# Kernel tuning notes

Hardware: AMD Instinct MI355X
Metric: run time of the kernel (lower is better)

Reference implementation:

```python
import jax, jax.numpy as jnp
import numpy as np

N_ENT = 100000
N_REL = 12
D = 64
E = 1000000
LAYER_DIMS = [64, 32]


def _xavier(key, shape):
    fan_in, fan_out = shape[-1], shape[-2] if len(shape) >= 2 else shape[-1]
    std = np.sqrt(2.0 / (fan_in + fan_out)).astype(np.float32)
    return jax.random.normal(key, shape, jnp.float32) * std


def setup_inputs() -> dict:
    key = jax.random.key(0)
    ks = jax.random.split(key, 14)
    return {
        "entity_emb": _xavier(ks[0], (N_ENT, D)),
        "rel_emb": _xavier(ks[1], (N_REL, D)),
        "W_r": _xavier(ks[2], (N_REL, D, D)),
        "W1_0_w": _xavier(ks[3], (LAYER_DIMS[0], D)),
        "W1_0_b": jnp.zeros((LAYER_DIMS[0],), jnp.float32),
        "W2_0_w": _xavier(ks[4], (LAYER_DIMS[0], D)),
        "W2_0_b": jnp.zeros((LAYER_DIMS[0],), jnp.float32),
        "W1_1_w": _xavier(ks[5], (LAYER_DIMS[1], LAYER_DIMS[0])),
        "W1_1_b": jnp.zeros((LAYER_DIMS[1],), jnp.float32),
        "W2_1_w": _xavier(ks[6], (LAYER_DIMS[1], LAYER_DIMS[0])),
        "W2_1_b": jnp.zeros((LAYER_DIMS[1],), jnp.float32),
        "src": jax.random.randint(ks[7], (E,), 0, N_ENT, jnp.int32),
        "dst": jax.random.randint(ks[8], (E,), 0, N_ENT, jnp.int32),
        "etype": jax.random.randint(ks[9], (E,), 0, N_REL, jnp.int32),
    }


def reference(entity_emb, rel_emb, W_r, W1_0_w, W1_0_b, W2_0_w, W2_0_b,
              W1_1_w, W1_1_b, W2_1_w, W2_1_b, src, dst, etype):
    n = entity_emb.shape[0]

    # --- compute_attention: per-edge TransR scores, edge_softmax over dst ---
    # Instead of gathering W_r[etype] per edge ([E,D,D] is huge), project every
    # node by every relation matrix once: [N, R, Dr].
    proj = jnp.einsum('nd,kdr->nkr', entity_emb, W_r)
    tail = proj[src, etype]          # [E, Dr] (src projected by its edge's W_r)
    head = proj[dst, etype]          # [E, Dr]
    rel = rel_emb[etype]             # [E, Dr]
    logits = jnp.sum(tail * jnp.tanh(head + rel), axis=-1)  # [E]

    # edge softmax grouped by destination node (stable)
    m = jax.ops.segment_max(logits, dst, num_segments=n)
    ex = jnp.exp(logits - m[dst])
    den = jax.ops.segment_sum(ex, dst, num_segments=n)
    att = ex / den[dst]              # [E]

    # --- KGATLayer: gather-scale-scatter + bi-interaction (dropout = 0) ---
    def layer(x, W1w, W1b, W2w, W2b):
        h_n = jax.ops.segment_sum(x[src] * att[:, None], dst, num_segments=n)
        add = jax.nn.leaky_relu((x + h_n) @ W1w.T + W1b)
        mul = jax.nn.leaky_relu((x * h_n) @ W2w.T + W2b)
        return add + mul

    x0 = entity_emb
    x1 = layer(x0, W1_0_w, W1_0_b, W2_0_w, W2_0_b)
    x2 = layer(x1, W1_1_w, W1_1_b, W2_1_w, W2_1_b)
    # embedder concatenates the input and every layer output
    return jnp.concatenate([x0, x1, x2], axis=1)  # [N, 64+64+32]
```

## Files before the change

kernel.cpp:

```cpp
#include <hip/hip_runtime.h>
#include <hip/hip_bf16.h>
#include <math.h>


typedef __attribute__((ext_vector_type(8))) short short8;
typedef __attribute__((ext_vector_type(4))) float float4v;

__device__ __forceinline__ short f2bf(float f) {
  __hip_bfloat16 h = __float2bfloat16(f);
  return *(short*)&h;
}
__device__ __forceinline__ float bf2f(short s) {
  return __uint_as_float(((unsigned)(unsigned short)s) << 16);
}

#define LOG2E 1.4426950408889634f
#define BS1_TILE 2048

__global__ void k_prep(const float* __restrict__ emb, short* __restrict__ emb_h,
                       float* __restrict__ out,
                       const float* __restrict__ Wr, short* __restrict__ Bt,
                       const float* __restrict__ W10, const float* __restrict__ W20,
                       const float* __restrict__ W11, const float* __restrict__ W21,
                       short* __restrict__ w1h0, short* __restrict__ w1l0,
                       short* __restrict__ w2h0, short* __restrict__ w2l0,
                       short* __restrict__ w1h1, short* __restrict__ w1l1,
                       short* __restrict__ w2h1, short* __restrict__ w2l1,
                       const int* __restrict__ src, const int* __restrict__ dst,
                       const int* __restrict__ et, int* __restrict__ bcur,
                       uint2* __restrict__ stg, int nE, int bsh, int cap,
                       int nb1, int nb_cvt, int n4) {
  __shared__ int hist[256];
  __shared__ int base[256];
  int b = blockIdx.x, t = threadIdx.x;
  if (b < nb1) {
    hist[t] = 0;
    __syncthreads();
    int tile = b * BS1_TILE;
#pragma unroll
    for (int j = 0; j < BS1_TILE / 256; j++) {
      int e = tile + j * 256 + t;
      if (e < nE) atomicAdd(&hist[dst[e] >> bsh], 1);
    }
    __syncthreads();
    int cnt = hist[t];
    if (cnt > 0) base[t] = atomicAdd(&bcur[t], cnt);
    hist[t] = 0;
    __syncthreads();
#pragma unroll
    for (int j = 0; j < BS1_TILE / 256; j++) {
      int e = tile + j * 256 + t;
      if (e < nE) {
        int d = dst[e], bk = d >> bsh;
        int r = atomicAdd(&hist[bk], 1);
        stg[(size_t)bk * cap + base[bk] + r] =
            make_uint2((unsigned)src[e], (unsigned)d | ((unsigned)et[e] << 20));
      }
    }
    return;
  }
  int b2 = b - nb1;
  if (b2 < nb_cvt) {
    int i = b2 * 256 + t;
    if (i < n4) {
      float4 v = ((const float4*)emb)[i];
      union { short s[4]; uint2 u; } o;
      o.s[0] = f2bf(v.x); o.s[1] = f2bf(v.y); o.s[2] = f2bf(v.z); o.s[3] = f2bf(v.w);
      ((uint2*)emb_h)[i] = o.u;
      int node = i >> 4, ch = i & 15;
      *(float4*)(out + (size_t)node * 160 + ch * 4) = v;
    }
  } else if (b2 < nb_cvt + 12) {
    int k = b2 - nb_cvt;
    for (int i = t; i < 4096; i += 256) {
      int d = i >> 6, r = i & 63;
      Bt[k * 4096 + r * 64 + d] = f2bf(Wr[k * 4096 + i]);
    }
  } else {
    int i = (b2 - nb_cvt - 12) * 256 + t;
    const float* W; short* H; short* L; int j;
    if (i < 4096) { W = W10; H = w1h0; L = w1l0; j = i; }
    else if (i < 8192) { W = W20; H = w2h0; L = w2l0; j = i - 4096; }
    else if (i < 10240) { W = W11; H = w1h1; L = w1l1; j = i - 8192; }
    else if (i < 12288) { W = W21; H = w2h1; L = w2l1; j = i - 10240; }
    else return;
    float w = W[j];
    short hi = f2bf(w);
    H[j] = hi;
    L[j] = f2bf(w - bf2f(hi));
  }
}

__global__ __launch_bounds__(256) void k_projb2(const short* __restrict__ A,
                                                const short* __restrict__ Bt,
                                                short* __restrict__ proj,
                                                int n_ent,
                                                const uint2* __restrict__ stg,
                                                const int* __restrict__ bcur,
                                                int* __restrict__ row_ptr,
                                                uint2* __restrict__ csr2,
                                                int nbg, int bsh, int cap,
                                                int nbuck, int nE) {
  __shared__ char smem[4 * 64 * 72 * 2];
  int bid = blockIdx.x, t = threadIdx.x;
  if (bid >= nbg) {
    int b = bid - nbg;
    int* cnt = (int*)smem;
    int* sc = cnt + 1024;
    int* bs = sc + 1024;
    int v = (t < nbuck) ? bcur[t] : 0;
    bs[t] = v;
    __syncthreads();
    for (int o = 1; o < 256; o <<= 1) {
      int a = (t >= o) ? bs[t - o] : 0;
      __syncthreads();
      bs[t] += a;
      __syncthreads();
    }
    int gbase = bs[b] - bcur[b];
    int n = n_ent;
    int lo = b << bsh;
    if (lo > n) lo = n;
    int hi = (b + 1) << bsh;
    if (hi > n) hi = n;
    int w = hi - lo;
#pragma unroll
    for (int j = 0; j < 4; j++) cnt[t + j * 256] = 0;
    __syncthreads();
    int m = bcur[b];
    const uint2* S = stg + (size_t)b * cap;
    for (int p = t; p < m; p += 256)
      atomicAdd(&cnt[(int)(S[p].y & 0xFFFFFu) - lo], 1);
    __syncthreads();
#pragma unroll
    for (int j = 0; j < 4; j++) sc[t + j * 256] = cnt[t + j * 256];
    __syncthreads();
    for (int o = 1; o < 1024; o <<= 1) {
      int a[4];
#pragma unroll
      for (int j = 0; j < 4; j++) {
        int i = t + j * 256;
        a[j] = (i >= o) ? sc[i - o] : 0;
      }
      __syncthreads();
#pragma unroll
      for (int j = 0; j < 4; j++) sc[t + j * 256] += a[j];
      __syncthreads();
    }
#pragma unroll
    for (int j = 0; j < 4; j++) {
      int i = t + j * 256;
      if (i < w) {
        int c0 = gbase + sc[i] - cnt[i];
        row_ptr[lo + i] = c0;
        cnt[i] = c0;
      }
    }
    if (b == nbuck - 1 && t == 0) row_ptr[n] = nE;
    __syncthreads();
    for (int p = t; p < m; p += 256) {
      uint2 vv = S[p];
      int d = (int)(vv.y & 0xFFFFFu);
      int pos = atomicAdd(&cnt[d - lo], 1);
      csr2[pos] = vv;
    }
    return;
  }
  int wave = t >> 6, lane = t & 63;
  int quad = lane >> 4, l16 = lane & 15;
  int m0 = bid * 256 + wave * 64;
  unsigned short* W = (unsigned short*)smem + wave * 64 * 72;
  short8 a[4][2];
#pragma unroll
  for (int mt = 0; mt < 4; mt++)
#pragma unroll
    for (int kc = 0; kc < 2; kc++) {
      int row = m0 + mt * 16 + l16;
      int rr = row < n_ent ? row : 0;
      a[mt][kc] = *(const short8*)(A + (size_t)rr * 64 + kc * 32 + quad * 8);
    }
  for (int k = 0; k < 12; k++) {
    const short* B = Bt + k * 4096;
    short8 b[4][2];
#pragma unroll
    for (int nt = 0; nt < 4; nt++)
#pragma unroll
      for (int kc = 0; kc < 2; kc++)
        b[nt][kc] = *(const short8*)(B + (nt * 16 + l16) * 64 + kc * 32 + quad * 8);
    float4v acc[4][4];
#pragma unroll
    for (int mt = 0; mt < 4; mt++)
#pragma unroll
      for (int nt = 0; nt < 4; nt++)
        acc[mt][nt] = (float4v){0.f, 0.f, 0.f, 0.f};
#pragma unroll
    for (int kc = 0; kc < 2; kc++)
#pragma unroll
      for (int mt = 0; mt < 4; mt++)
#pragma unroll
        for (int nt = 0; nt < 4; nt++)
          acc[mt][nt] = __builtin_amdgcn_mfma_f32_16x16x32_bf16(
              a[mt][kc], b[nt][kc], acc[mt][nt], 0, 0, 0);
#pragma unroll
    for (int mt = 0; mt < 4; mt++)
#pragma unroll
      for (int nt = 0; nt < 4; nt++)
#pragma unroll
        for (int r = 0; r < 4; r++) {
          int row = mt * 16 + quad * 4 + r;
          int col = nt * 16 + l16;
          W[row * 72 + col] = (unsigned short)f2bf(acc[mt][nt][r]);
        }
    const size_t plane = (size_t)k * n_ent;
#pragma unroll
    for (int i = 0; i < 8; i++) {
      int row = (lane >> 3) + 8 * i;
      int cs = (lane & 7) * 8;
      short8 v = *(const short8*)(W + row * 72 + cs);
      int node = m0 + row;
      if (node < n_ent)
        *(short8*)(proj + (plane + node) * 64 + cs) = v;
    }
  }
}

__global__ __launch_bounds__(256) void k_logits(const short* __restrict__ ps,
                                                const float* __restrict__ rel_emb,
                                                uint2* csr2, int nE, int n_ent) {
  int t = threadIdx.x;
  int lane = t & 63;
  int sub = lane >> 3;
  int c8 = (lane & 7) * 8;
  int e0 = (blockIdx.x * 4 + (t >> 6)) * 32;
  if (e0 >= nE) return;
  int ku[4];
  short8 tl[4], hd[4];
#pragma unroll
  for (int u = 0; u < 4; u++) {
    int e = e0 + u * 8 + sub;
    int ee = e < nE ? e : nE - 1;
    uint2 c = csr2[ee];
    int s = (int)c.x;
    int d = (int)(c.y & 0xFFFFFu);
    int k = (int)(c.y >> 20);
    ku[u] = k;
    const size_t plane = (size_t)k * n_ent;
    tl[u] = *(const short8*)(ps + (plane + s) * 64 + c8);
    hd[u] = *(const short8*)(ps + (plane + d) * 64 + c8);
  }
  float v[4];
#pragma unroll
  for (int u = 0; u < 4; u++) {
    const float* rp = rel_emb + ku[u] * 64 + c8;
    float4 r0 = *(const float4*)rp;
    float4 r1 = *(const float4*)(rp + 4);
    float rr[8] = {r0.x, r0.y, r0.z, r0.w, r1.x, r1.y, r1.z, r1.w};
    float vv = 0.f;
#pragma unroll
    for (int q = 0; q < 8; q++) {
      float x = bf2f(hd[u][q]) + rr[q];
      float tt = __builtin_amdgcn_exp2f(x * (2.f * LOG2E));
      float r = __builtin_amdgcn_rcpf(tt + 1.f);
      float th = fmaf(-2.f, r, 1.f);
      vv = fmaf(bf2f(tl[u][q]), th, vv);
    }
    vv += __shfl_xor(vv, 1);
    vv += __shfl_xor(vv, 2);
    vv += __shfl_xor(vv, 4);
    v[u] = __builtin_amdgcn_exp2f(vv * LOG2E);
  }
  int uu = lane & 7;
  if (uu < 4) {
    float myv = v[0];
    if (uu == 1) myv = v[1];
    if (uu == 2) myv = v[2];
    if (uu == 3) myv = v[3];
    int e = e0 + uu * 8 + sub;
    if (e < nE) csr2[e].y = __float_as_uint(myv);
  }
}

__global__ __launch_bounds__(256) void k_agg(const short* __restrict__ xh,
                                             const int* __restrict__ row_ptr,
                                             const uint2* __restrict__ csr,
                                             float* __restrict__ hn, int n_ent) {
  int wave = threadIdx.x >> 6, lane = threadIdx.x & 63;
  int n = blockIdx.x * 4 + wave;
  if (n >= n_ent) return;
  int jb = row_ptr[n], je = row_ptr[n + 1];
  int deg = je - jb;
  if (deg == 0) {
    hn[(size_t)n * 64 + lane] = 0.f;
    return;
  }
  uint2 c = (lane < deg) ? csr[jb + lane] : make_uint2(0u, 0u);
  int sidx = (int)c.x;
  float exv = (lane < deg) ? __uint_as_float(c.y) : 0.f;
  float den = exv;
#pragma unroll
  for (int o = 32; o; o >>= 1) den += __shfl_xor(den, o);
  int m = deg < 64 ? deg : 64;
  float acc = 0.f;
  for (int j = 0; j < m; j += 8) {
    int s0 = __shfl(sidx, j), s1 = __shfl(sidx, j + 1);
    int s2 = __shfl(sidx, j + 2), s3 = __shfl(sidx, j + 3);
    int s4 = __shfl(sidx, j + 4), s5 = __shfl(sidx, j + 5);
    int s6 = __shfl(sidx, j + 6), s7 = __shfl(sidx, j + 7);
    float e0 = __shfl(exv, j), e1 = __shfl(exv, j + 1);
    float e2 = __shfl(exv, j + 2), e3 = __shfl(exv, j + 3);
    float e4 = __shfl(exv, j + 4), e5 = __shfl(exv, j + 5);
    float e6 = __shfl(exv, j + 6), e7 = __shfl(exv, j + 7);
    short g0 = xh[(size_t)s0 * 64 + lane];
    short g1 = xh[(size_t)s1 * 64 + lane];
    short g2 = xh[(size_t)s2 * 64 + lane];
    short g3 = xh[(size_t)s3 * 64 + lane];
    short g4 = xh[(size_t)s4 * 64 + lane];
    short g5 = xh[(size_t)s5 * 64 + lane];
    short g6 = xh[(size_t)s6 * 64 + lane];
    short g7 = xh[(size_t)s7 * 64 + lane];
    acc = fmaf(e0, bf2f(g0), acc); acc = fmaf(e1, bf2f(g1), acc);
    acc = fmaf(e2, bf2f(g2), acc); acc = fmaf(e3, bf2f(g3), acc);
    acc = fmaf(e4, bf2f(g4), acc); acc = fmaf(e5, bf2f(g5), acc);
    acc = fmaf(e6, bf2f(g6), acc); acc = fmaf(e7, bf2f(g7), acc);
  }
  if (deg > 64) {
    for (int jj = jb + 64; jj < je; jj++) {
      uint2 cc = csr[jj];
      float ee = __uint_as_float(cc.y);
      den += ee;
      acc = fmaf(ee, bf2f(xh[(size_t)cc.x * 64 + lane]), acc);
    }
  }
  hn[(size_t)n * 64 + lane] = acc / den;
}

template <int OD, bool FIRST>
__global__ __launch_bounds__(256) void k_upmfma(const float* __restrict__ x,
                                                const float* __restrict__ hn,
                                                const short* __restrict__ g1h,
                                                const short* __restrict__ g1l,
                                                const short* __restrict__ g2h,
                                                const short* __restrict__ g2l,
                                                const float* __restrict__ b1,
                                                const float* __restrict__ b2,
                                                float* __restrict__ out,
                                                float* __restrict__ x_next,
                                                short* __restrict__ xh_next,
                                                int n_ent) {
  constexpr int NT = OD / 16;
  constexpr int S = (OD == 64) ? 66 : 34;
  __shared__ short wbuf[4 * OD * 72];
  short* w1h = wbuf;
  short* w1l = wbuf + OD * 72;
  short* w2h = wbuf + 2 * OD * 72;
  short* w2l = wbuf + 3 * OD * 72;
  int t = threadIdx.x;
  for (int i = t; i < OD * 16; i += 256) {
    int o = i >> 4, dq = (i & 15) * 4;
    *(uint2*)(w1h + o * 72 + dq) = *(const uint2*)(g1h + o * 64 + dq);
    *(uint2*)(w1l + o * 72 + dq) = *(const uint2*)(g1l + o * 64 + dq);
    *(uint2*)(w2h + o * 72 + dq) = *(const uint2*)(g2h + o * 64 + dq);
    *(uint2*)(w2l + o * 72 + dq) = *(const uint2*)(g2l + o * 64 + dq);
  }
  int wave = t >> 6, lane = t & 63;
  int quad = lane >> 4, l16 = lane & 15;
  int m0 = blockIdx.x * 128 + wave * 32;
  float4v accA[2][NT], accM[2][NT];
#pragma unroll
  for (int mt = 0; mt < 2; mt++)
#pragma unroll
    for (int nt = 0; nt < NT; nt++) {
      accA[mt][nt] = (float4v){0.f, 0.f, 0.f, 0.f};
      accM[mt][nt] = (float4v){0.f, 0.f, 0.f, 0.f};
    }
  __syncthreads();
#pragma unroll
  for (int kc = 0; kc < 2; kc++) {
    short8 ah_add[2], al_add[2], ah_mul[2], al_mul[2];
#pragma unroll
    for (int mt = 0; mt < 2; mt++) {
      int row = m0 + mt * 16 + l16;
      int rr = row < n_ent ? row : 0;
      const float* xp = x + (size_t)rr * 64 + kc * 32 + quad * 8;
      const float* hp = hn + (size_t)rr * 64 + kc * 32 + quad * 8;
      float4 xa = *(const float4*)xp;
      float4 xb = *(const float4*)(xp + 4);
      float4 ha = *(const float4*)hp;
      float4 hb = *(const float4*)(hp + 4);
      float xs[8] = {xa.x, xa.y, xa.z, xa.w, xb.x, xb.y, xb.z, xb.w};
      float hs[8] = {ha.x, ha.y, ha.z, ha.w, hb.x, hb.y, hb.z, hb.w};
#pragma unroll
      for (int q = 0; q < 8; q++) {
        float s = xs[q] + hs[q];
        short shi = f2bf(s);
        ah_add[mt][q] = shi;
        al_add[mt][q] = f2bf(s - bf2f(shi));
        float p = xs[q] * hs[q];
        short phi = f2bf(p);
        ah_mul[mt][q] = phi;
        al_mul[mt][q] = f2bf(p - bf2f(phi));
      }
    }
#pragma unroll
    for (int nt = 0; nt < NT; nt++) {
      int boff = (nt * 16 + l16) * 72 + kc * 32 + quad * 8;
      short8 b1h = *(const short8*)(w1h + boff);
      short8 b1l = *(const short8*)(w1l + boff);
      short8 b2h = *(const short8*)(w2h + boff);
      short8 b2l = *(const short8*)(w2l + boff);
#pragma unroll
      for (int mt = 0; mt < 2; mt++) {
        accA[mt][nt] = __builtin_amdgcn_mfma_f32_16x16x32_bf16(
            ah_add[mt], b1h, accA[mt][nt], 0, 0, 0);
        accA[mt][nt] = __builtin_amdgcn_mfma_f32_16x16x32_bf16(
            al_add[mt], b1h, accA[mt][nt], 0, 0, 0);
        accA[mt][nt] = __builtin_amdgcn_mfma_f32_16x16x32_bf16(
            ah_add[mt], b1l, accA[mt][nt], 0, 0, 0);
        accM[mt][nt] = __builtin_amdgcn_mfma_f32_16x16x32_bf16(
            ah_mul[mt], b2h, accM[mt][nt], 0, 0, 0);
        accM[mt][nt] = __builtin_amdgcn_mfma_f32_16x16x32_bf16(
            al_mul[mt], b2h, accM[mt][nt], 0, 0, 0);
        accM[mt][nt] = __builtin_amdgcn_mfma_f32_16x16x32_bf16(
            ah_mul[mt], b2l, accM[mt][nt], 0, 0, 0);
      }
    }
  }
  __syncthreads();
  float* yt = (float*)wbuf + wave * 32 * S;
#pragma unroll
  for (int nt = 0; nt < NT; nt++) {
    int col = nt * 16 + l16;
    float bb1 = b1[col], bb2 = b2[col];
#pragma unroll
    for (int mt = 0; mt < 2; mt++) {
#pragma unroll
      for (int r = 0; r < 4; r++) {
        float aa = accA[mt][nt][r] + bb1;
        float mm = accM[mt][nt][r] + bb2;
        aa = aa > 0.f ? aa : 0.01f * aa;
        mm = mm > 0.f ? mm : 0.01f * mm;
        yt[(mt * 16 + quad * 4 + r) * S + col] = aa + mm;
      }
    }
  }
  constexpr int LPR = OD / 4;
  constexpr int RPI = 64 / LPR;
#pragma unroll
  for (int i = 0; i < 32 / RPI; i++) {
    int rloc = i * RPI + lane / LPR;
    int c4 = (lane % LPR) * 4;
    float4 v = *(const float4*)(yt + rloc * S + c4);
    int node = m0 + rloc;
    if (node < n_ent) {
      if constexpr (FIRST) {
        *(float4*)(out + (size_t)node * 160 + 64 + c4) = v;
        *(float4*)(x_next + (size_t)node * 64 + c4) = v;
        unsigned p0 = (unsigned)(unsigned short)f2bf(v.x) |
                      ((unsigned)(unsigned short)f2bf(v.y) << 16);
        unsigned p1 = (unsigned)(unsigned short)f2bf(v.z) |
                      ((unsigned)(unsigned short)f2bf(v.w) << 16);
        *(uint2*)(xh_next + (size_t)node * 64 + c4) = make_uint2(p0, p1);
      } else {
        *(float4*)(out + (size_t)node * 160 + 128 + c4) = v;
      }
    }
  }
}

extern "C" void kernel_launch(void* const* d_in, const int* in_sizes, int n_in,
                              void* d_out, int out_size, void* d_ws, size_t ws_size,
                              hipStream_t stream) {
  const float* emb = (const float*)d_in[0];
  const float* rel = (const float*)d_in[1];
  const float* Wr = (const float*)d_in[2];
  const float* W10w = (const float*)d_in[3];
  const float* W10b = (const float*)d_in[4];
  const float* W20w = (const float*)d_in[5];
  const float* W20b = (const float*)d_in[6];
  const float* W11w = (const float*)d_in[7];
  const float* W11b = (const float*)d_in[8];
  const float* W21w = (const float*)d_in[9];
  const float* W21b = (const float*)d_in[10];
  const int* src = (const int*)d_in[11];
  const int* dst = (const int*)d_in[12];
  const int* et = (const int*)d_in[13];
  int N = in_sizes[0] / 64;
  int E = in_sizes[11];
  float* out = (float*)d_out;

  int bsh = 9;
  while (((N + (1 << bsh) - 1) >> bsh) > 256) bsh++;
  int nbuck = (N + (1 << bsh) - 1) >> bsh;
  int cap = ((E / nbuck) * 3 / 2 + 1024 + 255) / 256 * 256;

  char* p = (char*)d_ws;
  auto alloc = [&](size_t bytes) -> char* {
    char* r = p;
    p += (bytes + 255) / 256 * 256;
    return r;
  };
  short* proj = (short*)alloc((size_t)N * 768 * 2);
  uint2* csr2 = (uint2*)alloc((size_t)E * 8);
  uint2* stg = (uint2*)alloc((size_t)nbuck * cap * 8);
  int* row_ptr = (int*)alloc((size_t)(N + 1) * 4);
  int* bcur = (int*)alloc(1024);
  float* hn = (float*)alloc((size_t)N * 64 * 4);
  float* x1 = (float*)alloc((size_t)N * 64 * 4);
  short* emb_h = (short*)alloc(((size_t)N + 256) * 64 * 2);
  short* x1h = (short*)alloc(((size_t)N + 256) * 64 * 2);
  short* Bt = (short*)alloc((size_t)12 * 4096 * 2);
  short* w1h0 = (short*)alloc(4096 * 2);
  short* w1l0 = (short*)alloc(4096 * 2);
  short* w2h0 = (short*)alloc(4096 * 2);
  short* w2l0 = (short*)alloc(4096 * 2);
  short* w1h1 = (short*)alloc(2048 * 2);
  short* w1l1 = (short*)alloc(2048 * 2);
  short* w2h1 = (short*)alloc(2048 * 2);
  short* w2l1 = (short*)alloc(2048 * 2);

  int n4 = N * 16;
  int nb_cvt = (n4 + 255) / 256;
  int nb1 = (E + BS1_TILE - 1) / BS1_TILE;
  int nbg = (N + 255) / 256;

  hipMemsetAsync(bcur, 0, 1024, stream);
  k_prep<<<nb1 + nb_cvt + 60, 256, 0, stream>>>(
      emb, emb_h, out, Wr, Bt, W10w, W20w, W11w, W21w,
      w1h0, w1l0, w2h0, w2l0, w1h1, w1l1, w2h1, w2l1,
      src, dst, et, bcur, stg, E, bsh, cap, nb1, nb_cvt, n4);
  k_projb2<<<nbg + nbuck, 256, 0, stream>>>(
      emb_h, Bt, proj, N, stg, bcur, row_ptr, csr2, nbg, bsh, cap, nbuck, E);
  k_logits<<<(E + 127) / 128, 256, 0, stream>>>(proj, rel, csr2, E, N);
  k_agg<<<(N + 3) / 4, 256, 0, stream>>>(emb_h, row_ptr, csr2, hn, N);
  k_upmfma<64, true><<<(N + 127) / 128, 256, 0, stream>>>(
      emb, hn, w1h0, w1l0, w2h0, w2l0, W10b, W20b, out, x1, x1h, N);
  k_agg<<<(N + 3) / 4, 256, 0, stream>>>(x1h, row_ptr, csr2, hn, N);
  k_upmfma<32, false><<<(N + 127) / 128, 256, 0, stream>>>(
      x1, hn, w1h1, w1l1, w2h1, w2l1, W11b, W21b, out, nullptr, nullptr, N);
}
```

Measured before the change: 338.2 us.

## Double edges per wave in logits kernel and swizzle blocks across XCDs

```diff
diff --git a/kernel.cpp b/kernel.cpp
--- a/kernel.cpp
+++ b/kernel.cpp
@@ -226,17 +226,22 @@
 
 __global__ __launch_bounds__(256) void k_logits(const short* __restrict__ ps,
                                                 const float* __restrict__ rel_emb,
-                                                uint2* csr2, int nE, int n_ent) {
+                                                uint2* csr2, int nE, int n_ent,
+                                                int nwg) {
+  int bid = blockIdx.x;
+  int q = nwg >> 3, r8 = nwg & 7;
+  int xcd = bid & 7, idx = bid >> 3;
+  int swz = (xcd < r8 ? xcd * (q + 1) : r8 * (q + 1) + (xcd - r8) * q) + idx;
   int t = threadIdx.x;
   int lane = t & 63;
   int sub = lane >> 3;
   int c8 = (lane & 7) * 8;
-  int e0 = (blockIdx.x * 4 + (t >> 6)) * 32;
+  int e0 = (swz * 4 + (t >> 6)) * 64;
   if (e0 >= nE) return;
-  int ku[4];
-  short8 tl[4], hd[4];
-#pragma unroll
-  for (int u = 0; u < 4; u++) {
+  int ku[8];
+  short8 tl[8], hd[8];
+#pragma unroll
+  for (int u = 0; u < 8; u++) {
     int e = e0 + u * 8 + sub;
     int ee = e < nE ? e : nE - 1;
     uint2 c = csr2[ee];
@@ -248,21 +253,21 @@
     tl[u] = *(const short8*)(ps + (plane + s) * 64 + c8);
     hd[u] = *(const short8*)(ps + (plane + d) * 64 + c8);
   }
-  float v[4];
-#pragma unroll
-  for (int u = 0; u < 4; u++) {
+  float v[8];
+#pragma unroll
+  for (int u = 0; u < 8; u++) {
     const float* rp = rel_emb + ku[u] * 64 + c8;
     float4 r0 = *(const float4*)rp;
     float4 r1 = *(const float4*)(rp + 4);
     float rr[8] = {r0.x, r0.y, r0.z, r0.w, r1.x, r1.y, r1.z, r1.w};
     float vv = 0.f;
 #pragma unroll
-    for (int q = 0; q < 8; q++) {
-      float x = bf2f(hd[u][q]) + rr[q];
+    for (int qq = 0; qq < 8; qq++) {
+      float x = bf2f(hd[u][qq]) + rr[qq];
       float tt = __builtin_amdgcn_exp2f(x * (2.f * LOG2E));
-      float r = __builtin_amdgcn_rcpf(tt + 1.f);
-      float th = fmaf(-2.f, r, 1.f);
-      vv = fmaf(bf2f(tl[u][q]), th, vv);
+      float rc = __builtin_amdgcn_rcpf(tt + 1.f);
+      float th = fmaf(-2.f, rc, 1.f);
+      vv = fmaf(bf2f(tl[u][qq]), th, vv);
     }
     vv += __shfl_xor(vv, 1);
     vv += __shfl_xor(vv, 2);
@@ -270,14 +275,12 @@
     v[u] = __builtin_amdgcn_exp2f(vv * LOG2E);
   }
   int uu = lane & 7;
-  if (uu < 4) {
-    float myv = v[0];
-    if (uu == 1) myv = v[1];
-    if (uu == 2) myv = v[2];
-    if (uu == 3) myv = v[3];
-    int e = e0 + uu * 8 + sub;
-    if (e < nE) csr2[e].y = __float_as_uint(myv);
-  }
+  float myv = v[0];
+#pragma unroll
+  for (int u = 1; u < 8; u++)
+    if (uu == u) myv = v[u];
+  int e = e0 + uu * 8 + sub;
+  if (e < nE) csr2[e].y = __float_as_uint(myv);
 }
 
 __global__ __launch_bounds__(256) void k_agg(const short* __restrict__ xh,
@@ -390,15 +393,15 @@
       float xs[8] = {xa.x, xa.y, xa.z, xa.w, xb.x, xb.y, xb.z, xb.w};
       float hs[8] = {ha.x, ha.y, ha.z, ha.w, hb.x, hb.y, hb.z, hb.w};
 #pragma unroll
-      for (int q = 0; q < 8; q++) {
-        float s = xs[q] + hs[q];
+      for (int qq = 0; qq < 8; qq++) {
+        float s = xs[qq] + hs[qq];
         short shi = f2bf(s);
-        ah_add[mt][q] = shi;
-        al_add[mt][q] = f2bf(s - bf2f(shi));
-        float p = xs[q] * hs[q];
+        ah_add[mt][qq] = shi;
+        al_add[mt][qq] = f2bf(s - bf2f(shi));
+        float p = xs[qq] * hs[qq];
         short phi = f2bf(p);
-        ah_mul[mt][q] = phi;
-        al_mul[mt][q] = f2bf(p - bf2f(phi));
+        ah_mul[mt][qq] = phi;
+        al_mul[mt][qq] = f2bf(p - bf2f(phi));
       }
     }
 #pragma unroll
@@ -522,6 +525,7 @@
   int nb_cvt = (n4 + 255) / 256;
   int nb1 = (E + BS1_TILE - 1) / BS1_TILE;
   int nbg = (N + 255) / 256;
+  int nwg_lg = (E + 255) / 256;
 
   hipMemsetAsync(bcur, 0, 1024, stream);
   k_prep<<<nb1 + nb_cvt + 60, 256, 0, stream>>>(
@@ -530,7 +534,7 @@
       src, dst, et, bcur, stg, E, bsh, cap, nb1, nb_cvt, n4);
   k_projb2<<<nbg + nbuck, 256, 0, stream>>>(
       emb_h, Bt, proj, N, stg, bcur, row_ptr, csr2, nbg, bsh, cap, nbuck, E);
-  k_logits<<<(E + 127) / 128, 256, 0, stream>>>(proj, rel, csr2, E, N);
+  k_logits<<<nwg_lg, 256, 0, stream>>>(proj, rel, csr2, E, N, nwg_lg);
   k_agg<<<(N + 3) / 4, 256, 0, stream>>>(emb_h, row_ptr, csr2, hn, N);
   k_upmfma<64, true><<<(N + 127) / 128, 256, 0, stream>>>(
       emb, hn, w1h0, w1l0, w2h0, w2l0, W10b, W20b, out, x1, x1h, N);
```

New measurement: 335.6 us (median of 2 runs). No clear change (-0.8%).
